# Kernel optimization log

Hardware: AMD Instinct MI355X
Metric: run time of the kernel (lower is better)

Reference implementation:

```python
import jax, jax.numpy as jnp
import numpy as np


def setup_inputs() -> dict:
    key = jax.random.key(0)
    kq, kk, kv, kiq, kik = jax.random.split(key, 5)
    B, H, S, D = 2, 16, 4096, 64
    NSQ = 2048  # round(0.5 * S)
    NSK = 2048  # round(0.5 * S)
    Q = jax.random.normal(kq, (B, H, S, D), dtype=jnp.float32)
    K = jax.random.normal(kk, (B, H, S, D), dtype=jnp.float32)
    V = jax.random.normal(kv, (B, H, S, D), dtype=jnp.float32)
    mask = jnp.ones((B, S), dtype=jnp.float32)
    sample_idx_q = jnp.sort(jax.random.randint(kiq, (NSQ,), 0, S, dtype=jnp.int32))
    sample_idx_k = jax.random.randint(kik, (NSK,), 0, S, dtype=jnp.int32)
    return {"Q": Q, "K": K, "V": V, "mask": mask,
            "sample_idx_q": sample_idx_q, "sample_idx_k": sample_idx_k}


def reference(Q, K, V, mask, sample_idx_q, sample_idx_k):
    # Q,K,V: [B,H,S,D]; sample_idx_q sorted int [NSQ]; sample_idx_k int [NSK]
    S = Q.shape[-2]
    nsq = sample_idx_q.shape[0]
    nsk = sample_idx_k.shape[0]
    Qs = Q[:, :, sample_idx_q, :]            # [B,H,NSQ,D]
    Vs = V[:, :, sample_idx_k, :]            # [B,H,NSK,D]
    # NOTE: original code computes K's softmax from Q (faithful to source bug):
    Qsm = jax.nn.softmax(Qs, axis=-1)        # softmax over head_dim
    Ksm = jax.nn.softmax(Qsm, axis=-2)       # softmax over sampled seq dim
    # dot = K^T @ V : [B,H,D,D]  (requires NSQ == NSK, as in source)
    dot = jnp.einsum('bhsd,bhse->bhde', Ksm, Vs)
    ac = jnp.einsum('bhsd,bhde->bhse', Qsm, dot)  # [B,H,NSQ,D]
    scale = (S * S) / (nsq * nsk)
    ac = scale * ac + (S / nsk) * Vs
    # Serial duplicate-merge + scatter == segmented sum over duplicate q indices,
    # written into a zero tensor at the unique sampled positions.
    attn = jnp.zeros_like(V).at[:, :, sample_idx_q, :].add(ac)
    return attn
```

## Files before the change

### kernel.cpp

```cpp
#include <hip/hip_runtime.h>

constexpr int S    = 4096;
constexpr int D    = 64;
constexpr int NSQ  = 2048;
constexpr int BH   = 32;
constexpr int SD   = S * D;

constexpr int SPA  = 32;
constexpr int RPB  = NSQ / SPA;
constexpr int PEA  = 66;
constexpr int PQ   = 68;
constexpr int PAC  = 65;

using f32x16 = __attribute__((ext_vector_type(16))) float;
using s16x8  = __attribute__((ext_vector_type(8)))  short;

#define DEV static __device__ __forceinline__

DEV unsigned short f2bf(float f) {
    unsigned x = __builtin_bit_cast(unsigned, f);
    x += 0x7fffu + ((x >> 16) & 1u);
    return (unsigned short)(x >> 16);
}
DEV float bf2f(unsigned short u) {
    unsigned x = (unsigned)u << 16;
    return __builtin_bit_cast(float, x);
}
DEV s16x8 load_frag(const unsigned short* p) {
    const unsigned* u = (const unsigned*)p;
    union { unsigned w[4]; s16x8 v; } r;
    r.w[0] = u[0]; r.w[1] = u[1]; r.w[2] = u[2]; r.w[3] = u[3];
    return r.v;
}

__global__ __launch_bounds__(256) void
kA(const float* __restrict__ Q, const float* __restrict__ V,
   const int* __restrict__ iq, const int* __restrict__ ik,
   float* __restrict__ Mp, float* __restrict__ Cp,
   unsigned short* __restrict__ Qsw, unsigned short* __restrict__ Vsw) {
    __shared__ unsigned short Et[64 * PEA];
    __shared__ unsigned short Vt[64 * PEA];
    __shared__ float Cl[4][256];
    __shared__ int iqL[RPB], ikL[RPB];

    const int bh   = blockIdx.x / SPA;
    const int sp   = blockIdx.x % SPA;
    const int lane = threadIdx.x & 63;
    const int wave = threadIdx.x >> 6;
    const int rq   = lane >> 4;
    const int c    = lane & 15;
    const int rbase = sp * RPB;

    if (threadIdx.x < RPB) {
        iqL[threadIdx.x] = iq[rbase + threadIdx.x];
        ikL[threadIdx.x] = ik[rbase + threadIdx.x];
    }
    __syncthreads();

    const float* Qb = Q + (size_t)bh * SD;
    const float* Vb = V + (size_t)bh * SD;

    float c4[4] = {0.f, 0.f, 0.f, 0.f};
    #pragma unroll
    for (int it = 0; it < 4; ++it) {
        const int sl = wave * 16 + it * 4 + rq;
        const int qi = iqL[sl];
        const int ki = ikL[sl];
        const float4 qv = *(const float4*)&Qb[qi * D + 4 * c];
        const float4 vv = *(const float4*)&Vb[ki * D + 4 * c];
        const float e0 = __expf(qv.x), e1 = __expf(qv.y),
                    e2 = __expf(qv.z), e3 = __expf(qv.w);
        float s = (e0 + e1) + (e2 + e3);
        s += __shfl_xor(s, 1); s += __shfl_xor(s, 2);
        s += __shfl_xor(s, 4); s += __shfl_xor(s, 8);
        const float inv = 1.0f / s;
        const float q0 = e0 * inv, q1 = e1 * inv, q2 = e2 * inv, q3 = e3 * inv;
        const float E0 = __expf(q0), E1 = __expf(q1),
                    E2 = __expf(q2), E3 = __expf(q3);
        c4[0] += E0; c4[1] += E1; c4[2] += E2; c4[3] += E3;
        Et[(4 * c + 0) * PEA + sl] = f2bf(E0);
        Et[(4 * c + 1) * PEA + sl] = f2bf(E1);
        Et[(4 * c + 2) * PEA + sl] = f2bf(E2);
        Et[(4 * c + 3) * PEA + sl] = f2bf(E3);
        Vt[(4 * c + 0) * PEA + sl] = f2bf(vv.x);
        Vt[(4 * c + 1) * PEA + sl] = f2bf(vv.y);
        Vt[(4 * c + 2) * PEA + sl] = f2bf(vv.z);
        Vt[(4 * c + 3) * PEA + sl] = f2bf(vv.w);
        uint2 pk;
        pk.x = (unsigned)f2bf(q0) | ((unsigned)f2bf(q1) << 16);
        pk.y = (unsigned)f2bf(q2) | ((unsigned)f2bf(q3) << 16);
        *(uint2*)&Qsw[((size_t)bh * NSQ + rbase + sl) * 64 + 4 * c] = pk;
        uint2 pv;
        pv.x = (unsigned)f2bf(vv.x) | ((unsigned)f2bf(vv.y) << 16);
        pv.y = (unsigned)f2bf(vv.z) | ((unsigned)f2bf(vv.w) << 16);
        *(uint2*)&Vsw[((size_t)bh * NSQ + rbase + sl) * 64 + 4 * c] = pv;
    }
    Cl[wave][lane * 4 + 0] = c4[0];
    Cl[wave][lane * 4 + 1] = c4[1];
    Cl[wave][lane * 4 + 2] = c4[2];
    Cl[wave][lane * 4 + 3] = c4[3];
    __syncthreads();

    const int m = lane & 31, h = lane >> 5;
    const int d0 = (wave & 1) * 32, n0 = (wave >> 1) * 32;
    f32x16 acc = {0,0,0,0,0,0,0,0,0,0,0,0,0,0,0,0};
    #pragma unroll
    for (int t = 0; t < RPB / 16; ++t) {
        s16x8 a = load_frag(&Et[(d0 + m) * PEA + t * 16 + h * 8]);
        s16x8 b = load_frag(&Vt[(n0 + m) * PEA + t * 16 + h * 8]);
        acc = __builtin_amdgcn_mfma_f32_32x32x16_bf16(a, b, acc, 0, 0, 0);
    }
    float* Mb = Mp + ((size_t)bh * SPA + sp) * 4096;
    #pragma unroll
    for (int r = 0; r < 16; ++r) {
        const int row = (r & 3) + 8 * (r >> 2) + 4 * h;
        Mb[(d0 + row) * 64 + n0 + m] = acc[r];
    }
    if (wave == 0) {
        const int cc = lane >> 2, j = lane & 3;
        float cs = 0.f;
        #pragma unroll
        for (int w = 0; w < 4; ++w)
            #pragma unroll
            for (int r = 0; r < 4; ++r)
                cs += Cl[w][(16 * r + cc) * 4 + j];
        Cp[((size_t)bh * SPA + sp) * 64 + lane] = cs;
    }
}

__global__ __launch_bounds__(256) void
kB(const float* __restrict__ Mp, const float* __restrict__ Cp,
   unsigned short* __restrict__ Gtw) {
    __shared__ float Cf[64];
    const int bh = blockIdx.x >> 2;
    const int qr = blockIdx.x & 3;

    if (threadIdx.x < 64) {
        float cs = 0.f;
        #pragma unroll 8
        for (int p = 0; p < SPA; ++p)
            cs += Cp[((size_t)bh * SPA + p) * 64 + threadIdx.x];
        Cf[threadIdx.x] = cs;
    }
    __syncthreads();

    const int l = qr * 1024 + threadIdx.x * 4;
    const int d = l >> 6;
    const float* MpB = Mp + (size_t)bh * SPA * 4096;
    float4 ms = {0.f, 0.f, 0.f, 0.f};
    #pragma unroll 8
    for (int p = 0; p < SPA; ++p) {
        const float4 t = *(const float4*)&MpB[p * 4096 + l];
        ms.x += t.x; ms.y += t.y; ms.z += t.z; ms.w += t.w;
    }
    const float g = 4.0f / Cf[d];
    uint2 pk;
    pk.x = (unsigned)f2bf(ms.x * g) | ((unsigned)f2bf(ms.y * g) << 16);
    pk.y = (unsigned)f2bf(ms.z * g) | ((unsigned)f2bf(ms.w * g) << 16);
    *(uint2*)&Gtw[(size_t)bh * 4096 + l] = pk;
}

__global__ __launch_bounds__(256) void
kC(const int* __restrict__ iq,
   const unsigned short* __restrict__ Qsw, const unsigned short* __restrict__ Vsw,
   const unsigned short* __restrict__ Gtw, float* __restrict__ out) {
    __shared__ __align__(16) char smem[RPB * PQ * 2 + 64 * PQ * 2];
    unsigned short* Qs = (unsigned short*)smem;
    unsigned short* Gt = (unsigned short*)(smem + RPB * PQ * 2);
    float*          Ac = (float*)smem;
    __shared__ int iqL[RPB];

    const int bh   = blockIdx.x / SPA;
    const int sp   = blockIdx.x % SPA;
    const int lane = threadIdx.x & 63;
    const int wave = threadIdx.x >> 6;
    const int rbase = sp * RPB;

    if (threadIdx.x < RPB) iqL[threadIdx.x] = iq[rbase + threadIdx.x];

    {
        const int l0 = threadIdx.x * 16;
        const int d  = l0 >> 6, e0 = l0 & 63;
        const uint4 w0 = *(const uint4*)&Gtw[(size_t)bh * 4096 + l0];
        const uint4 w1 = *(const uint4*)&Gtw[(size_t)bh * 4096 + l0 + 8];
        const unsigned wv[8] = {w0.x, w0.y, w0.z, w0.w, w1.x, w1.y, w1.z, w1.w};
        #pragma unroll
        for (int j = 0; j < 8; ++j) {
            Gt[(e0 + 2 * j + 0) * PQ + d] = (unsigned short)(wv[j] & 0xffffu);
            Gt[(e0 + 2 * j + 1) * PQ + d] = (unsigned short)(wv[j] >> 16);
        }
    }
    {
        const int l0  = threadIdx.x * 16;
        const int row = l0 >> 6, col = l0 & 63;
        const unsigned short* src = &Qsw[((size_t)bh * NSQ + rbase) * 64 + l0];
        const uint4 w0 = *(const uint4*)src;
        const uint4 w1 = *(const uint4*)(src + 8);
        *(uint2*)&Qs[row * PQ + col + 0]  = make_uint2(w0.x, w0.y);
        *(uint2*)&Qs[row * PQ + col + 4]  = make_uint2(w0.z, w0.w);
        *(uint2*)&Qs[row * PQ + col + 8]  = make_uint2(w1.x, w1.y);
        *(uint2*)&Qs[row * PQ + col + 12] = make_uint2(w1.z, w1.w);
    }
    __syncthreads();

    const int m0 = (wave & 1) * 32, n0 = (wave >> 1) * 32;
    const int m  = lane & 31, h = lane >> 5;
    f32x16 acc = {0,0,0,0,0,0,0,0,0,0,0,0,0,0,0,0};
    #pragma unroll
    for (int t = 0; t < RPB / 16; ++t) {
        s16x8 a = load_frag(&Qs[(m0 + m) * PQ + t * 16 + h * 8]);
        s16x8 b = load_frag(&Gt[(n0 + m) * PQ + t * 16 + h * 8]);
        acc = __builtin_amdgcn_mfma_f32_32x32x16_bf16(a, b, acc, 0, 0, 0);
    }
    __syncthreads();

    #pragma unroll
    for (int r = 0; r < 16; ++r) {
        const int row = (r & 3) + 8 * (r >> 2) + 4 * h;
        Ac[(m0 + row) * PAC + n0 + m] = acc[r];
    }
    __syncthreads();

    const int r  = threadIdx.x >> 2;
    const int c0 = (threadIdx.x & 3) * 16;
    const int qi = iqL[r];
    const bool leader = (r == 0) || (iqL[r - 1] != qi);
    if (leader) {
        float sum[16];
        #pragma unroll
        for (int k = 0; k < 16; ++k) sum[k] = 0.f;
        const unsigned short* Vblk = Vsw + ((size_t)bh * NSQ + rbase) * 64;
        int j = r;
        for (; j < RPB && iqL[j] == qi; ++j) {
            const float* ar = &Ac[j * PAC + c0];
            #pragma unroll
            for (int k = 0; k < 16; ++k) sum[k] += ar[k];
            const uint4 w0 = *(const uint4*)&Vblk[(size_t)j * 64 + c0];
            const uint4 w1 = *(const uint4*)&Vblk[(size_t)j * 64 + c0 + 8];
            const unsigned wv[8] = {w0.x, w0.y, w0.z, w0.w, w1.x, w1.y, w1.z, w1.w};
            #pragma unroll
            for (int k2 = 0; k2 < 8; ++k2) {
                sum[2 * k2 + 0] += 2.0f * bf2f((unsigned short)(wv[k2] & 0xffffu));
                sum[2 * k2 + 1] += 2.0f * bf2f((unsigned short)(wv[k2] >> 16));
            }
        }
        const int gPrev = (rbase == 0)        ? -1 : iq[rbase - 1];
        const int gNext = (rbase + RPB == NSQ) ? -1 : iq[rbase + RPB];
        const bool edge = (r == 0 && qi == gPrev) || (j == RPB && qi == gNext);
        float* dst = out + (size_t)bh * SD + (size_t)qi * D + c0;
        if (!edge) {
            #pragma unroll
            for (int k4 = 0; k4 < 4; ++k4)
                *(float4*)&dst[4 * k4] = make_float4(sum[4 * k4 + 0], sum[4 * k4 + 1],
                                                     sum[4 * k4 + 2], sum[4 * k4 + 3]);
        } else {
            #pragma unroll
            for (int k = 0; k < 16; ++k) atomicAdd(&dst[k], sum[k]);
        }
    }
}

extern "C" void kernel_launch(void* const* d_in, const int* in_sizes, int n_in,
                              void* d_out, int out_size, void* d_ws, size_t ws_size,
                              hipStream_t stream) {
    const float* Q  = (const float*)d_in[0];
    const float* V  = (const float*)d_in[2];
    const int*   iq = (const int*)d_in[4];
    const int*   ik = (const int*)d_in[5];
    float*       out = (float*)d_out;

    float*          Mp  = (float*)d_ws;
    float*          Cp  = Mp + (size_t)BH * SPA * 4096;
    unsigned short* Qsw = (unsigned short*)(Cp + (size_t)BH * SPA * 64);
    unsigned short* Vsw = Qsw + (size_t)BH * NSQ * 64;
    unsigned short* Gtw = Vsw + (size_t)BH * NSQ * 64;

    kA<<<BH * SPA, 256, 0, stream>>>(Q, V, iq, ik, Mp, Cp, Qsw, Vsw);
    kB<<<BH * 4, 256, 0, stream>>>(Mp, Cp, Gtw);
    kC<<<BH * SPA, 256, 0, stream>>>(iq, Qsw, Vsw, Gtw, out);
}
```

Measured before the change: 146.7 us.

## Drop bf16 Vs workspace; gather V in kC into MFMA accumulator init

kA no longer writes a bf16 copy of the sampled V rows. kC instead gathers the fp32 V rows through sample_idx_k and seeds the MFMA accumulator with 2*V, so the residual term is added inside the matmul rather than in the scatter loop. Block index mapping is also swapped so consecutive blocks cover different heads instead of splits of the same head. This removes one workspace write and read pass, at the cost of scattered fp32 gathers in kC, which also raises the precision of the V term.

```diff
diff --git a/kernel.cpp b/kernel.cpp
--- a/kernel.cpp
+++ b/kernel.cpp
@@ -22,10 +22,6 @@
     x += 0x7fffu + ((x >> 16) & 1u);
     return (unsigned short)(x >> 16);
 }
-DEV float bf2f(unsigned short u) {
-    unsigned x = (unsigned)u << 16;
-    return __builtin_bit_cast(float, x);
-}
 DEV s16x8 load_frag(const unsigned short* p) {
     const unsigned* u = (const unsigned*)p;
     union { unsigned w[4]; s16x8 v; } r;
@@ -37,14 +33,14 @@
 kA(const float* __restrict__ Q, const float* __restrict__ V,
    const int* __restrict__ iq, const int* __restrict__ ik,
    float* __restrict__ Mp, float* __restrict__ Cp,
-   unsigned short* __restrict__ Qsw, unsigned short* __restrict__ Vsw) {
+   unsigned short* __restrict__ Qsw) {
     __shared__ unsigned short Et[64 * PEA];
     __shared__ unsigned short Vt[64 * PEA];
     __shared__ float Cl[4][256];
     __shared__ int iqL[RPB], ikL[RPB];
 
-    const int bh   = blockIdx.x / SPA;
-    const int sp   = blockIdx.x % SPA;
+    const int bh   = blockIdx.x & 31;
+    const int sp   = blockIdx.x >> 5;
     const int lane = threadIdx.x & 63;
     const int wave = threadIdx.x >> 6;
     const int rq   = lane >> 4;
@@ -90,10 +86,6 @@
         pk.x = (unsigned)f2bf(q0) | ((unsigned)f2bf(q1) << 16);
         pk.y = (unsigned)f2bf(q2) | ((unsigned)f2bf(q3) << 16);
         *(uint2*)&Qsw[((size_t)bh * NSQ + rbase + sl) * 64 + 4 * c] = pk;
-        uint2 pv;
-        pv.x = (unsigned)f2bf(vv.x) | ((unsigned)f2bf(vv.y) << 16);
-        pv.y = (unsigned)f2bf(vv.z) | ((unsigned)f2bf(vv.w) << 16);
-        *(uint2*)&Vsw[((size_t)bh * NSQ + rbase + sl) * 64 + 4 * c] = pv;
     }
     Cl[wave][lane * 4 + 0] = c4[0];
     Cl[wave][lane * 4 + 1] = c4[1];
@@ -132,8 +124,8 @@
 kB(const float* __restrict__ Mp, const float* __restrict__ Cp,
    unsigned short* __restrict__ Gtw) {
     __shared__ float Cf[64];
-    const int bh = blockIdx.x >> 2;
-    const int qr = blockIdx.x & 3;
+    const int bh = blockIdx.x & 31;
+    const int qr = blockIdx.x >> 5;
 
     if (threadIdx.x < 64) {
         float cs = 0.f;
@@ -161,22 +153,25 @@
 }
 
 __global__ __launch_bounds__(256) void
-kC(const int* __restrict__ iq,
-   const unsigned short* __restrict__ Qsw, const unsigned short* __restrict__ Vsw,
-   const unsigned short* __restrict__ Gtw, float* __restrict__ out) {
+kC(const float* __restrict__ V, const int* __restrict__ iq, const int* __restrict__ ik,
+   const unsigned short* __restrict__ Qsw, const unsigned short* __restrict__ Gtw,
+   float* __restrict__ out) {
     __shared__ __align__(16) char smem[RPB * PQ * 2 + 64 * PQ * 2];
     unsigned short* Qs = (unsigned short*)smem;
     unsigned short* Gt = (unsigned short*)(smem + RPB * PQ * 2);
     float*          Ac = (float*)smem;
-    __shared__ int iqL[RPB];
-
-    const int bh   = blockIdx.x / SPA;
-    const int sp   = blockIdx.x % SPA;
+    __shared__ int iqL[RPB], ikL[RPB];
+
+    const int bh   = blockIdx.x & 31;
+    const int sp   = blockIdx.x >> 5;
     const int lane = threadIdx.x & 63;
     const int wave = threadIdx.x >> 6;
     const int rbase = sp * RPB;
 
-    if (threadIdx.x < RPB) iqL[threadIdx.x] = iq[rbase + threadIdx.x];
+    if (threadIdx.x < RPB) {
+        iqL[threadIdx.x] = iq[rbase + threadIdx.x];
+        ikL[threadIdx.x] = ik[rbase + threadIdx.x];
+    }
 
     {
         const int l0 = threadIdx.x * 16;
@@ -205,7 +200,14 @@
 
     const int m0 = (wave & 1) * 32, n0 = (wave >> 1) * 32;
     const int m  = lane & 31, h = lane >> 5;
-    f32x16 acc = {0,0,0,0,0,0,0,0,0,0,0,0,0,0,0,0};
+    const float* Vb = V + (size_t)bh * SD;
+    f32x16 acc;
+    #pragma unroll
+    for (int r = 0; r < 16; ++r) {
+        const int row = (r & 3) + 8 * (r >> 2) + 4 * h;
+        const int ki  = ikL[m0 + row];
+        acc[r] = 2.0f * Vb[ki * D + n0 + m];
+    }
     #pragma unroll
     for (int t = 0; t < RPB / 16; ++t) {
         s16x8 a = load_frag(&Qs[(m0 + m) * PQ + t * 16 + h * 8]);
@@ -229,22 +231,13 @@
         float sum[16];
         #pragma unroll
         for (int k = 0; k < 16; ++k) sum[k] = 0.f;
-        const unsigned short* Vblk = Vsw + ((size_t)bh * NSQ + rbase) * 64;
         int j = r;
         for (; j < RPB && iqL[j] == qi; ++j) {
             const float* ar = &Ac[j * PAC + c0];
             #pragma unroll
             for (int k = 0; k < 16; ++k) sum[k] += ar[k];
-            const uint4 w0 = *(const uint4*)&Vblk[(size_t)j * 64 + c0];
-            const uint4 w1 = *(const uint4*)&Vblk[(size_t)j * 64 + c0 + 8];
-            const unsigned wv[8] = {w0.x, w0.y, w0.z, w0.w, w1.x, w1.y, w1.z, w1.w};
-            #pragma unroll
-            for (int k2 = 0; k2 < 8; ++k2) {
-                sum[2 * k2 + 0] += 2.0f * bf2f((unsigned short)(wv[k2] & 0xffffu));
-                sum[2 * k2 + 1] += 2.0f * bf2f((unsigned short)(wv[k2] >> 16));
-            }
         }
-        const int gPrev = (rbase == 0)        ? -1 : iq[rbase - 1];
+        const int gPrev = (rbase == 0)         ? -1 : iq[rbase - 1];
         const int gNext = (rbase + RPB == NSQ) ? -1 : iq[rbase + RPB];
         const bool edge = (r == 0 && qi == gPrev) || (j == RPB && qi == gNext);
         float* dst = out + (size_t)bh * SD + (size_t)qi * D + c0;
@@ -272,10 +265,9 @@
     float*          Mp  = (float*)d_ws;
     float*          Cp  = Mp + (size_t)BH * SPA * 4096;
     unsigned short* Qsw = (unsigned short*)(Cp + (size_t)BH * SPA * 64);
-    unsigned short* Vsw = Qsw + (size_t)BH * NSQ * 64;
-    unsigned short* Gtw = Vsw + (size_t)BH * NSQ * 64;
-
-    kA<<<BH * SPA, 256, 0, stream>>>(Q, V, iq, ik, Mp, Cp, Qsw, Vsw);
+    unsigned short* Gtw = Qsw + (size_t)BH * NSQ * 64;
+
+    kA<<<BH * SPA, 256, 0, stream>>>(Q, V, iq, ik, Mp, Cp, Qsw);
     kB<<<BH * 4, 256, 0, stream>>>(Mp, Cp, Gtw);
-    kC<<<BH * SPA, 256, 0, stream>>>(iq, Qsw, Vsw, Gtw, out);
-}
+    kC<<<BH * SPA, 256, 0, stream>>>(V, iq, ik, Qsw, Gtw, out);
+}
```

Result: no change. 145.7 us (-0.7%).
